# Performance work log

Measured on AMD Instinct MI355X. Metric: run time of the kernel, lower is better.

Reference implementation:

```python
import jax, jax.numpy as jnp
import numpy as np

NUM_INPUTS = 45056
NUM_OUTPUTS = 1032  # L1 (1024) + psqt buckets (8)
MAX_ACTIVE = 32
BATCH = 4096


def setup_inputs() -> dict:
    key = jax.random.key(0)
    k0, k1, kw, kb = jax.random.split(key, 4)
    feature_indices_0 = jax.random.randint(k0, (BATCH, MAX_ACTIVE), 0, NUM_INPUTS, dtype=jnp.int64 if jax.config.jax_enable_x64 else jnp.int32)
    feature_indices_1 = jax.random.randint(k1, (BATCH, MAX_ACTIVE), 0, NUM_INPUTS, dtype=jnp.int64 if jax.config.jax_enable_x64 else jnp.int32)
    feature_values_0 = jnp.ones((BATCH, MAX_ACTIVE), dtype=jnp.float32)
    feature_values_1 = jnp.ones((BATCH, MAX_ACTIVE), dtype=jnp.float32)
    sigma = float(np.sqrt(1.0 / NUM_INPUTS))
    merged_weight = jax.random.normal(kw, (NUM_INPUTS, NUM_OUTPUTS), dtype=jnp.float32) * sigma
    bias = jax.random.uniform(kb, (NUM_OUTPUTS,), dtype=jnp.float32, minval=-sigma, maxval=sigma)
    return {
        'feature_indices_0': feature_indices_0,
        'feature_values_0': feature_values_0,
        'feature_indices_1': feature_indices_1,
        'feature_values_1': feature_values_1,
        'merged_weight': merged_weight,
        'bias': bias,
    }


def _sparse_linear(indices, values, weight, bias):
    # Gather active-feature rows [B, K, D], accumulate weighted by values, add bias.
    rows = jnp.take(weight, indices, axis=0)          # [B, K, D]
    return bias + jnp.einsum('bk,bkd->bd', values, rows)  # [B, D]


def reference(feature_indices_0, feature_values_0, feature_indices_1, feature_values_1, merged_weight, bias):
    out0 = _sparse_linear(feature_indices_0, feature_values_0, merged_weight, bias)
    out1 = _sparse_linear(feature_indices_1, feature_values_1, merged_weight, bias)
    return out0, out1
```

## Files before the change

### kernel.cpp

```cpp
#include <hip/hip_runtime.h>


#define BATCH 4096
#define MAX_ACTIVE 32
#define DIM 1032
#define DIM4 258

__global__ __launch_bounds__(256) void ft_gather_kernel(
    const int* __restrict__ idx0, const float* __restrict__ val0,
    const int* __restrict__ idx1, const float* __restrict__ val1,
    const float* __restrict__ W, const float* __restrict__ bias,
    float* __restrict__ out)
{
    const int b   = blockIdx.x;
    const int set = b >> 12;
    const int row = b & (BATCH - 1);

    const int*   idx = set ? idx1 : idx0;
    const float* val = set ? val1 : val0;

    __shared__ int   s_idx[MAX_ACTIVE];
    __shared__ float s_val[MAX_ACTIVE];

    const int t = threadIdx.x;
    if (t < MAX_ACTIVE) {
        s_idx[t] = idx[row * MAX_ACTIVE + t];
        s_val[t] = val[row * MAX_ACTIVE + t];
    }
    __syncthreads();

    float* outp = out + (size_t)b * DIM;

    for (int c = t; c < DIM4; c += 256) {
        float4 acc = ((const float4*)bias)[c];
        #pragma unroll 8
        for (int k = 0; k < MAX_ACTIVE; ++k) {
            const float4 w = ((const float4*)(W + (size_t)s_idx[k] * DIM))[c];
            const float v = s_val[k];
            acc.x += v * w.x;
            acc.y += v * w.y;
            acc.z += v * w.z;
            acc.w += v * w.w;
        }
        ((float4*)outp)[c] = acc;
    }
}

extern "C" void kernel_launch(void* const* d_in, const int* in_sizes, int n_in,
                              void* d_out, int out_size, void* d_ws, size_t ws_size,
                              hipStream_t stream) {
    const int*   idx0 = (const int*)d_in[0];
    const float* val0 = (const float*)d_in[1];
    const int*   idx1 = (const int*)d_in[2];
    const float* val1 = (const float*)d_in[3];
    const float* W    = (const float*)d_in[4];
    const float* bias = (const float*)d_in[5];
    float* out = (float*)d_out;

    dim3 grid(2 * BATCH);
    dim3 block(256);
    ft_gather_kernel<<<grid, block, 0, stream>>>(idx0, val0, idx1, val1, W, bias, out);
}
```

Baseline: 384.7 us.

## Convert weights to fp16 in workspace and gather half-precision rows

Each call first converts the full f32 weight matrix into an fp16 copy in the workspace. A new gather kernel then reads 16-byte fp16 chunks, 8 outputs per thread, and accumulates in f32. It handles two batch rows per block, issues 8 row loads back to back, and uses readfirstlane to keep indices and values scalar. This halves the bytes fetched by the random row gather, at the cost of a full read and write of the weights every call and reduced weight precision. If the workspace is too small, it falls back to the original f32 kernel.

Measured after the change: 365.8 us. 1.05x faster.

```diff
diff --git a/kernel.cpp b/kernel.cpp
--- a/kernel.cpp
+++ b/kernel.cpp
@@ -1,12 +1,86 @@
 #include <hip/hip_runtime.h>
+#include <hip/hip_fp16.h>
 
 
+#define NUM_INPUTS 45056
 #define BATCH 4096
 #define MAX_ACTIVE 32
 #define DIM 1032
-#define DIM4 258
+#define CHUNKS 129
+#define W_ELEMS ((size_t)NUM_INPUTS * (size_t)DIM)
 
-__global__ __launch_bounds__(256) void ft_gather_kernel(
+__device__ __forceinline__ float uniform_f(float x) {
+    return __int_as_float(__builtin_amdgcn_readfirstlane(__float_as_int(x)));
+}
+
+__global__ __launch_bounds__(256) void convert_w_f16(
+    const float* __restrict__ W, __half2* __restrict__ Wh2)
+{
+    const size_t n4 = W_ELEMS / 4;
+    const size_t stride = (size_t)gridDim.x * blockDim.x;
+    for (size_t i = (size_t)blockIdx.x * blockDim.x + threadIdx.x; i < n4; i += stride) {
+        const float4 w = ((const float4*)W)[i];
+        Wh2[2 * i]     = __floats2half2_rn(w.x, w.y);
+        Wh2[2 * i + 1] = __floats2half2_rn(w.z, w.w);
+    }
+}
+
+__global__ __launch_bounds__(256) void ft_gather_f16(
+    const int* __restrict__ idx0, const float* __restrict__ val0,
+    const int* __restrict__ idx1, const float* __restrict__ val1,
+    const __half* __restrict__ Wh, const float* __restrict__ bias,
+    float* __restrict__ out)
+{
+    const int which = threadIdx.x >> 7;
+    const int u     = threadIdx.x & 127;
+    const int rt    = 2 * blockIdx.x + which;
+    const int set   = rt >> 12;
+    const int row   = rt & (BATCH - 1);
+
+    __shared__ int   s_idx[2][MAX_ACTIVE];
+    __shared__ float s_val[2][MAX_ACTIVE];
+
+    if (u < MAX_ACTIVE) {
+        const int*   idx = set ? idx1 : idx0;
+        const float* val = set ? val1 : val0;
+        s_idx[which][u] = idx[row * MAX_ACTIVE + u];
+        s_val[which][u] = val[row * MAX_ACTIVE + u];
+    }
+    __syncthreads();
+
+    float* outp = out + (size_t)rt * DIM;
+
+    for (int c = u; c < CHUNKS; c += 128) {
+        const float* bp = bias + 8 * c;
+        float4 acc0 = ((const float4*)bp)[0];
+        float4 acc1 = ((const float4*)bp)[1];
+
+        for (int k0 = 0; k0 < MAX_ACTIVE; k0 += 8) {
+            uint4 w[8];
+            #pragma unroll
+            for (int j = 0; j < 8; ++j) {
+                const int i = __builtin_amdgcn_readfirstlane(s_idx[which][k0 + j]);
+                w[j] = ((const uint4*)(Wh + (size_t)i * DIM))[c];
+            }
+            #pragma unroll
+            for (int j = 0; j < 8; ++j) {
+                const float v = uniform_f(s_val[which][k0 + j]);
+                const float2 f0 = __half22float2(*(const __half2*)&w[j].x);
+                const float2 f1 = __half22float2(*(const __half2*)&w[j].y);
+                const float2 f2 = __half22float2(*(const __half2*)&w[j].z);
+                const float2 f3 = __half22float2(*(const __half2*)&w[j].w);
+                acc0.x += v * f0.x;  acc0.y += v * f0.y;
+                acc0.z += v * f1.x;  acc0.w += v * f1.y;
+                acc1.x += v * f2.x;  acc1.y += v * f2.y;
+                acc1.z += v * f3.x;  acc1.w += v * f3.y;
+            }
+        }
+        ((float4*)(outp + 8 * c))[0] = acc0;
+        ((float4*)(outp + 8 * c))[1] = acc1;
+    }
+}
+
+__global__ __launch_bounds__(256) void ft_gather_f32(
     const int* __restrict__ idx0, const float* __restrict__ val0,
     const int* __restrict__ idx1, const float* __restrict__ val1,
     const float* __restrict__ W, const float* __restrict__ bias,
@@ -15,13 +89,11 @@
     const int b   = blockIdx.x;
     const int set = b >> 12;
     const int row = b & (BATCH - 1);
-
     const int*   idx = set ? idx1 : idx0;
     const float* val = set ? val1 : val0;
 
     __shared__ int   s_idx[MAX_ACTIVE];
     __shared__ float s_val[MAX_ACTIVE];
-
     const int t = threadIdx.x;
     if (t < MAX_ACTIVE) {
         s_idx[t] = idx[row * MAX_ACTIVE + t];
@@ -30,17 +102,14 @@
     __syncthreads();
 
     float* outp = out + (size_t)b * DIM;
-
-    for (int c = t; c < DIM4; c += 256) {
+    for (int c = t; c < DIM / 4 + (DIM % 4 != 0); c += 256) {
         float4 acc = ((const float4*)bias)[c];
         #pragma unroll 8
         for (int k = 0; k < MAX_ACTIVE; ++k) {
             const float4 w = ((const float4*)(W + (size_t)s_idx[k] * DIM))[c];
             const float v = s_val[k];
-            acc.x += v * w.x;
-            acc.y += v * w.y;
-            acc.z += v * w.z;
-            acc.w += v * w.w;
+            acc.x += v * w.x; acc.y += v * w.y;
+            acc.z += v * w.z; acc.w += v * w.w;
         }
         ((float4*)outp)[c] = acc;
     }
@@ -57,7 +126,12 @@
     const float* bias = (const float*)d_in[5];
     float* out = (float*)d_out;
 
-    dim3 grid(2 * BATCH);
-    dim3 block(256);
-    ft_gather_kernel<<<grid, block, 0, stream>>>(idx0, val0, idx1, val1, W, bias, out);
+    const size_t need = W_ELEMS * sizeof(__half);
+    if (ws_size >= need) {
+        __half* Wh = (__half*)d_ws;
+        convert_w_f16<<<4096, 256, 0, stream>>>(W, (__half2*)Wh);
+        ft_gather_f16<<<BATCH, 256, 0, stream>>>(idx0, val0, idx1, val1, Wh, bias, out);
+    } else {
+        ft_gather_f32<<<2 * BATCH, 256, 0, stream>>>(idx0, val0, idx1, val1, W, bias, out);
+    }
 }
```
